# Kernel optimization log

Measured on AMD Instinct MI355X. Metric: run time of the kernel, lower is better.

Reference implementation:

```python
import jax, jax.numpy as jnp
import numpy as np

N_NODES = 100000
N_EDGES = 1600000
D = 64
LN_EPS = 1e-5


def gcn_layer(x, src, dst, adv, W, b, g, be):
    # message: softmax(log(adv), dst) == adv / segment_sum(adv)[dst]  (per-target-node normalization)
    denom = jax.ops.segment_sum(adv, dst, num_segments=N_NODES)  # [N]
    att = adv / denom[dst]                                       # [E]
    msg = x[src] * att[:, None]                                  # [E, D] gather-multiply
    aggr = jax.ops.segment_sum(msg, dst, num_segments=N_NODES)   # [N, D] scatter-add
    # update: LayerNorm(Dropout(Linear(gelu(aggr) + x)))  (dropout = identity in eval)
    h = jax.nn.gelu(aggr, approximate=False) + x
    h = h @ W + b
    mu = jnp.mean(h, axis=-1, keepdims=True)
    var = jnp.mean((h - mu) ** 2, axis=-1, keepdims=True)
    return (h - mu) * jax.lax.rsqrt(var + LN_EPS) * g + be


def setup_inputs() -> dict:
    key = jax.random.key(0)
    ks = jax.random.split(key, 8)
    scale = 1.0 / np.sqrt(D)
    node_attr = jax.random.normal(ks[0], (N_NODES, D), jnp.float32)
    edge_index = jax.random.randint(ks[1], (2, N_EDGES), 0, N_NODES)
    batch_idx = jnp.zeros((N_NODES,), jnp.int32)
    adv_att0 = jax.random.uniform(ks[2], (N_EDGES,), jnp.float32) + 1e-3
    adv_att1 = jax.random.uniform(ks[3], (N_EDGES,), jnp.float32) + 1e-3
    W0 = jax.random.uniform(ks[4], (D, D), jnp.float32, -scale, scale)
    W1 = jax.random.uniform(ks[5], (D, D), jnp.float32, -scale, scale)
    b0 = jnp.zeros((D,), jnp.float32)
    b1 = jnp.zeros((D,), jnp.float32)
    g0 = jnp.ones((D,), jnp.float32)
    g1 = jnp.ones((D,), jnp.float32)
    be0 = jnp.zeros((D,), jnp.float32)
    be1 = jnp.zeros((D,), jnp.float32)
    return {"node_attr": node_attr, "edge_index": edge_index, "batch_idx": batch_idx,
            "adv_att0": adv_att0, "adv_att1": adv_att1,
            "W0": W0, "b0": b0, "g0": g0, "be0": be0,
            "W1": W1, "b1": b1, "g1": g1, "be1": be1}


def reference(node_attr, edge_index, batch_idx, adv_att0, adv_att1,
              W0, b0, g0, be0, W1, b1, g1, be1):
    src = edge_index[0]  # j (source)
    dst = edge_index[1]  # i (target)
    h = gcn_layer(node_attr, src, dst, adv_att0, W0, b0, g0, be0)
    h = gcn_layer(h, src, dst, adv_att1, W1, b1, g1, be1)
    return h  # node_level=True -> per-node representations [N, D]
```

## Files before the change

### kernel.cpp

```cpp
#include <hip/hip_runtime.h>
#include <math.h>

#define N_NODES 100000
#define N_EDGES 1600000
#define D 64
#define LN_EPS 1e-5f
#define NQ (N_EDGES / 4)
#define NODE_RANGE 12500
#define CAP 48

typedef int v2i __attribute__((ext_vector_type(2)));
typedef int v4i __attribute__((ext_vector_type(4)));
typedef float v2f __attribute__((ext_vector_type(2)));

__device__ __forceinline__ unsigned short f2b(float f) {
    unsigned u = __float_as_uint(f);
    return (unsigned short)((u + 0x7FFFu + ((u >> 16) & 1u)) >> 16);
}
__device__ __forceinline__ unsigned pk2(float lo, float hi) {
    return (unsigned)f2b(lo) | ((unsigned)f2b(hi) << 16);
}
__device__ __forceinline__ float b2f(unsigned short u) {
    return __uint_as_float((unsigned)u << 16);
}

__global__ void k_tobf16z(const float4* __restrict__ in4, uint4* __restrict__ out4,
                          int* __restrict__ cnt) {
    int i = blockIdx.x * 256 + threadIdx.x;
    if (i < N_NODES) cnt[i] = 0;
    float4 a = in4[2 * i];
    float4 c = in4[2 * i + 1];
    uint4 o;
    o.x = pk2(a.x, a.y);
    o.y = pk2(a.z, a.w);
    o.z = pk2(c.x, c.y);
    o.w = pk2(c.z, c.w);
    out4[i] = o;
}

__global__ void k_bucket(const int* __restrict__ src, const v4i* __restrict__ dst4,
                         const float* __restrict__ adv0, const float* __restrict__ adv1,
                         int* __restrict__ cnt, v2i* __restrict__ rec) {
    const int g = blockIdx.x & 7;
    const int lb = blockIdx.x >> 3;
    const int nlb = gridDim.x >> 3;
    const int lo = g * NODE_RANGE, hi = lo + NODE_RANGE;
    for (int q = lb * 256 + threadIdx.x; q < NQ; q += nlb * 256) {
        v4i d = dst4[q];
        int e = q * 4;
#pragma unroll
        for (int c = 0; c < 4; ++c) {
            int dd = (c == 0) ? d.x : (c == 1) ? d.y : (c == 2) ? d.z : d.w;
            if (dd >= lo && dd < hi) {
                int p = atomicAdd(&cnt[dd], 1);
                if (p < CAP) {
                    int s = src[e + c];
                    float a0 = adv0[e + c];
                    float a1 = adv1[e + c];
                    v2i r;
                    r.x = s;
                    r.y = (int)pk2(a0, a1);
                    __builtin_nontemporal_store(r, &rec[(size_t)p * N_NODES + dd]);
                }
            }
        }
    }
}

template <int LAYER>
__global__ __launch_bounds__(256) void k_layer(const float* __restrict__ xres,
                                               const unsigned short* __restrict__ xb,
                                               const v2i* __restrict__ rec,
                                               const int* __restrict__ cnt,
                                               const float* __restrict__ W,
                                               const float* __restrict__ bb,
                                               const float* __restrict__ gg,
                                               const float* __restrict__ be,
                                               float* __restrict__ outf,
                                               unsigned short* __restrict__ outb) {
    const int lane = threadIdx.x & 63;
    const int wid = threadIdx.x >> 6;
    const int nodeA = blockIdx.x * 8 + wid;
    const int nodeB = nodeA + 4;
    const int nA = min(cnt[nodeA], CAP);
    const int nB = min(cnt[nodeB], CAP);

    const int slot = lane >> 3;
    const int fgrp = lane & 7;
    const int bpbase = slot << 2;

    __shared__ float shmem[4][2][8][66];
    __shared__ float hs[8][D];

    v2f accA[4], accB[4];
#pragma unroll
    for (int i = 0; i < 4; ++i) { accA[i] = (v2f)0.f; accB[i] = (v2f)0.f; }

    int svA = 0, aviA = 0, svB = 0, aviB = 0;
    if (lane < nA) {
        v2i r = rec[(size_t)lane * N_NODES + nodeA];
        svA = r.x;
        unsigned pa = (unsigned)r.y;
        aviA = (int)(LAYER ? (pa & 0xFFFF0000u) : (pa << 16));
    }
    if (lane < nB) {
        v2i r = rec[(size_t)lane * N_NODES + nodeB];
        svB = r.x;
        unsigned pa = (unsigned)r.y;
        aviB = (int)(LAYER ? (pa & 0xFFFF0000u) : (pa << 16));
    }
    float sadvA = __int_as_float(aviA);
    float sadvB = __int_as_float(aviB);

    const int nmax = max(nA, nB);
    for (int j0 = 0; j0 < nmax; j0 += 8) {
        const int idx = (j0 << 2) + bpbase;
        if (j0 < nA) {
            int s = __builtin_amdgcn_ds_bpermute(idx, svA);
            float a = __int_as_float(__builtin_amdgcn_ds_bpermute(idx, aviA));
            v2f av = {a, a};
            uint4 u = *(const uint4*)(xb + (unsigned)s * D + (fgrp << 3));
            v2f x0 = {__uint_as_float(u.x << 16), __uint_as_float(u.x & 0xFFFF0000u)};
            v2f x1 = {__uint_as_float(u.y << 16), __uint_as_float(u.y & 0xFFFF0000u)};
            v2f x2 = {__uint_as_float(u.z << 16), __uint_as_float(u.z & 0xFFFF0000u)};
            v2f x3 = {__uint_as_float(u.w << 16), __uint_as_float(u.w & 0xFFFF0000u)};
            accA[0] = __builtin_elementwise_fma(x0, av, accA[0]);
            accA[1] = __builtin_elementwise_fma(x1, av, accA[1]);
            accA[2] = __builtin_elementwise_fma(x2, av, accA[2]);
            accA[3] = __builtin_elementwise_fma(x3, av, accA[3]);
        }
        if (j0 < nB) {
            int s = __builtin_amdgcn_ds_bpermute(idx, svB);
            float a = __int_as_float(__builtin_amdgcn_ds_bpermute(idx, aviB));
            v2f av = {a, a};
            uint4 u = *(const uint4*)(xb + (unsigned)s * D + (fgrp << 3));
            v2f x0 = {__uint_as_float(u.x << 16), __uint_as_float(u.x & 0xFFFF0000u)};
            v2f x1 = {__uint_as_float(u.y << 16), __uint_as_float(u.y & 0xFFFF0000u)};
            v2f x2 = {__uint_as_float(u.z << 16), __uint_as_float(u.z & 0xFFFF0000u)};
            v2f x3 = {__uint_as_float(u.w << 16), __uint_as_float(u.w & 0xFFFF0000u)};
            accB[0] = __builtin_elementwise_fma(x0, av, accB[0]);
            accB[1] = __builtin_elementwise_fma(x1, av, accB[1]);
            accB[2] = __builtin_elementwise_fma(x2, av, accB[2]);
            accB[3] = __builtin_elementwise_fma(x3, av, accB[3]);
        }
    }

    {
        float* scA = &shmem[wid][0][slot][0];
        float* scB = &shmem[wid][1][slot][0];
#pragma unroll
        for (int i = 0; i < 4; ++i) {
            *(v2f*)&scA[fgrp * 8 + 2 * i] = accA[i];
            *(v2f*)&scB[fgrp * 8 + 2 * i] = accB[i];
        }
    }
    float sumA = 0.f, sumB = 0.f;
    {
        const float* rA = &shmem[wid][0][0][0];
        const float* rB = &shmem[wid][1][0][0];
#pragma unroll
        for (int s = 0; s < 8; ++s) {
            sumA += rA[s * 66 + lane];
            sumB += rB[s * 66 + lane];
        }
    }
    for (int m = 32; m; m >>= 1) {
        sadvA += __shfl_xor(sadvA, m, 64);
        sadvB += __shfl_xor(sadvB, m, 64);
    }
    float aggrA = (nA > 0) ? sumA / sadvA : 0.f;
    float aggrB = (nB > 0) ? sumB / sadvB : 0.f;

    float xvA = (LAYER == 0) ? xres[(unsigned)(nodeA * D) + lane]
                             : b2f(xb[(unsigned)(nodeA * D) + lane]);
    float xvB = (LAYER == 0) ? xres[(unsigned)(nodeB * D) + lane]
                             : b2f(xb[(unsigned)(nodeB * D) + lane]);
    float geA = 0.5f * aggrA;
    float geB = 0.5f * aggrB;
    hs[wid][lane] = fmaf(geA, erff(aggrA * 0.70710678118654752f), geA + xvA);
    hs[4 + wid][lane] = fmaf(geB, erff(aggrB * 0.70710678118654752f), geB + xvB);
    __syncthreads();

    float py[8];
#pragma unroll
    for (int i = 0; i < 8; ++i) py[i] = 0.f;
    const float* wp = W + (wid * 16) * D + lane;
#pragma unroll
    for (int k4 = 0; k4 < 4; ++k4) {
        float w0 = wp[(k4 * 4 + 0) * D];
        float w1 = wp[(k4 * 4 + 1) * D];
        float w2 = wp[(k4 * 4 + 2) * D];
        float w3 = wp[(k4 * 4 + 3) * D];
#pragma unroll
        for (int nn = 0; nn < 8; ++nn) {
            float4 hv = *(const float4*)&hs[nn][wid * 16 + k4 * 4];
            py[nn] = fmaf(hv.x, w0, fmaf(hv.y, w1, fmaf(hv.z, w2, fmaf(hv.w, w3, py[nn]))));
        }
    }
    {
        float* ppw = &shmem[wid][0][0][0];
#pragma unroll
        for (int nn = 0; nn < 8; ++nn) ppw[nn * 66 + lane] = py[nn];
    }
    __syncthreads();

    const float bl = bb[lane], gl = gg[lane], bel = be[lane];
#pragma unroll
    for (int half = 0; half < 2; ++half) {
        const int row = wid + half * 4;
        const int node = blockIdx.x * 8 + row;
        float acc2 = bl + (((&shmem[0][0][0][0])[row * 66 + lane] +
                            (&shmem[1][0][0][0])[row * 66 + lane]) +
                           ((&shmem[2][0][0][0])[row * 66 + lane] +
                            (&shmem[3][0][0][0])[row * 66 + lane]));
        float s = acc2;
        for (int m = 32; m; m >>= 1) s += __shfl_xor(s, m, 64);
        float mu = s * (1.f / 64.f);
        float dv = acc2 - mu;
        float v2 = dv * dv;
        for (int m = 32; m; m >>= 1) v2 += __shfl_xor(v2, m, 64);
        float var = v2 * (1.f / 64.f);
        float res = dv * rsqrtf(var + LN_EPS) * gl + bel;
        if (LAYER == 0)
            outb[(unsigned)(node * D) + lane] = f2b(res);
        else
            __builtin_nontemporal_store(res, outf + (unsigned)(node * D) + lane);
    }
}

extern "C" void kernel_launch(void* const* d_in, const int* in_sizes, int n_in,
                              void* d_out, int out_size, void* d_ws, size_t ws_size,
                              hipStream_t stream) {
    const float* node_attr = (const float*)d_in[0];
    const int* edge_index = (const int*)d_in[1];
    const float* adv0 = (const float*)d_in[3];
    const float* adv1 = (const float*)d_in[4];
    const float* W0 = (const float*)d_in[5];
    const float* b0 = (const float*)d_in[6];
    const float* g0 = (const float*)d_in[7];
    const float* be0 = (const float*)d_in[8];
    const float* W1 = (const float*)d_in[9];
    const float* b1 = (const float*)d_in[10];
    const float* g1 = (const float*)d_in[11];
    const float* be1 = (const float*)d_in[12];

    const int* src = edge_index;
    const v4i* dst4 = (const v4i*)(edge_index + N_EDGES);

    v2i* rec = (v2i*)d_ws;
    unsigned short* h1b = (unsigned short*)(rec + (size_t)N_NODES * CAP);
    int* cnt = (int*)(h1b + (size_t)N_NODES * D);

    float* out = (float*)d_out;
    unsigned short* xb0 = (unsigned short*)d_out;

    k_tobf16z<<<3125, 256, 0, stream>>>((const float4*)node_attr, (uint4*)xb0, cnt);

    k_bucket<<<4096, 256, 0, stream>>>(src, dst4, adv0, adv1, cnt, rec);

    k_layer<0><<<N_NODES / 8, 256, 0, stream>>>(node_attr, xb0, rec, cnt,
                                                W0, b0, g0, be0, nullptr, h1b);
    k_layer<1><<<N_NODES / 8, 256, 0, stream>>>(nullptr, h1b, rec, cnt,
                                                W1, b1, g1, be1, out, nullptr);
}
```

Baseline: 202.9 us.

## Split edge bucketing into slot-reservation and coalesced-fill kernels

The single bucketing kernel, where each block filtered all edges for one of 8 node ranges, is replaced by two passes. The first assigns slots with one atomic per edge and writes the slot positions to a temporary buffer that reuses h1b. The second reads src and attention values with vectorized loads and scatters the packed records. This removes the 8x redundant reading of dst and the scalar gathers, at the cost of an extra launch and a round trip through the position buffer. It also drops the node-range locality of the atomics and scattered stores that the old grouping may have provided.

```diff
diff --git a/kernel.cpp b/kernel.cpp
--- a/kernel.cpp
+++ b/kernel.cpp
@@ -6,7 +6,6 @@
 #define D 64
 #define LN_EPS 1e-5f
 #define NQ (N_EDGES / 4)
-#define NODE_RANGE 12500
 #define CAP 48
 
 typedef int v2i __attribute__((ext_vector_type(2)));
@@ -38,33 +37,34 @@
     out4[i] = o;
 }
 
-__global__ void k_bucket(const int* __restrict__ src, const v4i* __restrict__ dst4,
-                         const float* __restrict__ adv0, const float* __restrict__ adv1,
-                         int* __restrict__ cnt, v2i* __restrict__ rec) {
-    const int g = blockIdx.x & 7;
-    const int lb = blockIdx.x >> 3;
-    const int nlb = gridDim.x >> 3;
-    const int lo = g * NODE_RANGE, hi = lo + NODE_RANGE;
-    for (int q = lb * 256 + threadIdx.x; q < NQ; q += nlb * 256) {
-        v4i d = dst4[q];
-        int e = q * 4;
-#pragma unroll
-        for (int c = 0; c < 4; ++c) {
-            int dd = (c == 0) ? d.x : (c == 1) ? d.y : (c == 2) ? d.z : d.w;
-            if (dd >= lo && dd < hi) {
-                int p = atomicAdd(&cnt[dd], 1);
-                if (p < CAP) {
-                    int s = src[e + c];
-                    float a0 = adv0[e + c];
-                    float a1 = adv1[e + c];
-                    v2i r;
-                    r.x = s;
-                    r.y = (int)pk2(a0, a1);
-                    __builtin_nontemporal_store(r, &rec[(size_t)p * N_NODES + dd]);
-                }
-            }
-        }
-    }
+__global__ void k_pos(const v4i* __restrict__ dst4, int* __restrict__ cnt,
+                      v4i* __restrict__ pos4) {
+    int q = blockIdx.x * 256 + threadIdx.x;
+    if (q >= NQ) return;
+    v4i d = dst4[q];
+    v4i o;
+    int p;
+    p = atomicAdd(&cnt[d.x], 1); o.x = (p < CAP) ? p * N_NODES + d.x : -1;
+    p = atomicAdd(&cnt[d.y], 1); o.y = (p < CAP) ? p * N_NODES + d.y : -1;
+    p = atomicAdd(&cnt[d.z], 1); o.z = (p < CAP) ? p * N_NODES + d.z : -1;
+    p = atomicAdd(&cnt[d.w], 1); o.w = (p < CAP) ? p * N_NODES + d.w : -1;
+    pos4[q] = o;
+}
+
+__global__ void k_fill(const v4i* __restrict__ pos4, const v4i* __restrict__ src4,
+                       const float4* __restrict__ adv04, const float4* __restrict__ adv14,
+                       v2i* __restrict__ rec) {
+    int q = blockIdx.x * 256 + threadIdx.x;
+    if (q >= NQ) return;
+    v4i p = pos4[q];
+    v4i s = src4[q];
+    float4 a0 = adv04[q];
+    float4 a1 = adv14[q];
+    v2i r;
+    if (p.x >= 0) { r.x = s.x; r.y = (int)pk2(a0.x, a1.x); __builtin_nontemporal_store(r, &rec[p.x]); }
+    if (p.y >= 0) { r.x = s.y; r.y = (int)pk2(a0.y, a1.y); __builtin_nontemporal_store(r, &rec[p.y]); }
+    if (p.z >= 0) { r.x = s.z; r.y = (int)pk2(a0.z, a1.z); __builtin_nontemporal_store(r, &rec[p.z]); }
+    if (p.w >= 0) { r.x = s.w; r.y = (int)pk2(a0.w, a1.w); __builtin_nontemporal_store(r, &rec[p.w]); }
 }
 
 template <int LAYER>
@@ -244,19 +244,23 @@
     const float* g1 = (const float*)d_in[11];
     const float* be1 = (const float*)d_in[12];
 
-    const int* src = edge_index;
+    const v4i* src4 = (const v4i*)edge_index;
     const v4i* dst4 = (const v4i*)(edge_index + N_EDGES);
+    const float4* adv04 = (const float4*)adv0;
+    const float4* adv14 = (const float4*)adv1;
 
     v2i* rec = (v2i*)d_ws;
     unsigned short* h1b = (unsigned short*)(rec + (size_t)N_NODES * CAP);
     int* cnt = (int*)(h1b + (size_t)N_NODES * D);
+    v4i* pos4 = (v4i*)h1b;
 
     float* out = (float*)d_out;
     unsigned short* xb0 = (unsigned short*)d_out;
 
     k_tobf16z<<<3125, 256, 0, stream>>>((const float4*)node_attr, (uint4*)xb0, cnt);
 
-    k_bucket<<<4096, 256, 0, stream>>>(src, dst4, adv0, adv1, cnt, rec);
+    k_pos<<<(NQ + 255) / 256, 256, 0, stream>>>(dst4, cnt, pos4);
+    k_fill<<<(NQ + 255) / 256, 256, 0, stream>>>(pos4, src4, adv04, adv14, rec);
 
     k_layer<0><<<N_NODES / 8, 256, 0, stream>>>(node_attr, xb0, rec, cnt,
                                                 W0, b0, g0, be0, nullptr, h1b);
```

Result: slower. 238.6 us (+17.6%).
